# Optimization experiments

Measured on AMD Instinct MI355X. Metric: run time of the kernel, lower is better.

## Reference

```python
import jax, jax.numpy as jnp
import numpy as np

SIZE = 256  # output image is SIZE x SIZE


def lookup_table(size):
    # matches torch.meshgrid(indexing='ij') + stack + rot90
    lin = jnp.linspace(-1.0, 1.0, size)
    xx, yy = jnp.meshgrid(lin, lin, indexing='ij')
    t = jnp.stack([xx, yy], axis=-1)
    return jnp.rot90(t, 1, axes=(0, 1))  # [S,S,2]


def area2d(a, b, c):
    return (b[..., 0] - a[..., 0]) * (c[..., 1] - a[..., 1]) - (b[..., 1] - a[..., 1]) * (c[..., 0] - a[..., 0])


def face_normals(tris):
    n = jnp.cross(tris[:, 1] - tris[:, 0], tris[:, 2] - tris[:, 0])
    # NB: faithful to source: normalize by GLOBAL Frobenius norm (not per-face)
    return n / jnp.linalg.norm(n)


def vertex_normals(vertices, f):
    fn = face_normals(vertices[f])
    vn = jnp.zeros_like(vertices)
    vn = vn.at[f[:, 0]].add(fn).at[f[:, 1]].add(fn).at[f[:, 2]].add(fn)
    return vn / jnp.linalg.norm(vn)


def bilinear_sample(img, gx, gy):
    # torch.grid_sampler_2d, mode=bilinear, padding=zeros, align_corners=False
    # img: [C,H,W]; gx -> width axis, gy -> height axis, both in [-1,1]
    C, H, W = img.shape
    x = ((gx + 1.0) * W - 1.0) * 0.5
    y = ((gy + 1.0) * H - 1.0) * 0.5
    x0 = jnp.floor(x)
    y0 = jnp.floor(y)
    x1 = x0 + 1.0
    y1 = y0 + 1.0
    wx1 = x - x0
    wx0 = 1.0 - wx1
    wy1 = y - y0
    wy0 = 1.0 - wy1

    def gather(ix, iy):
        valid = (ix >= 0) & (ix <= W - 1) & (iy >= 0) & (iy <= H - 1)
        ixc = jnp.clip(ix, 0, W - 1).astype(jnp.int32)
        iyc = jnp.clip(iy, 0, H - 1).astype(jnp.int32)
        return img[:, iyc, ixc] * valid  # [C,...]

    return (gather(x0, y0) * (wx0 * wy0) + gather(x1, y0) * (wx1 * wy0)
            + gather(x0, y1) * (wx0 * wy1) + gather(x1, y1) * (wx1 * wy1))


def setup_inputs() -> dict:
    key = jax.random.key(0)
    k1, k2, k3, k4, k5, k6 = jax.random.split(key, 6)
    V, F, M = 1024, 256, 1024
    xy = jax.random.uniform(k1, (V, 2), minval=-1.0, maxval=1.0, dtype=jnp.float32)
    z = jax.random.uniform(k2, (V, 1), minval=0.5, maxval=1.5, dtype=jnp.float32)
    vertices = jnp.concatenate([xy, z], axis=1)
    faces = jax.random.randint(k3, (F, 3), 0, V, dtype=jnp.int64)
    uv = jax.random.uniform(k4, (M, 2), dtype=jnp.float32)
    uvfaces = jax.random.randint(k5, (F, 3), 0, M, dtype=jnp.int64)
    uvmap = jax.random.uniform(k6, (3, 256, 256), dtype=jnp.float32)
    return {"vertices": vertices, "faces": faces, "uv": uv, "uvfaces": uvfaces, "uvmap": uvmap}


def reference(vertices, faces, uv, uvfaces, uvmap):
    size = SIZE
    pts = lookup_table(size)                       # [S,S,2]
    uvn = uv * 2.0 - 1.0                            # init: uv*2-1
    tris = vertices[faces]                          # [F,3,3]
    z_inv = 1.0 / tris[:, :, 2:3]                   # [F,3,1]
    vn = vertex_normals(vertices, faces)[faces] * z_inv
    uvs = uvn[uvfaces] * z_inv
    tri9 = jnp.concatenate([tris, uvs, vn, z_inv], axis=2)  # [F,3,9]
    cullmask = face_normals(tris)[:, 2] > 0         # backface cull, eye=(0,0,1)

    t2 = tris[:, :, :2]
    A = area2d(t2[:, 0], t2[:, 1], t2[:, 2])        # [F] signed double-area
    valid_tri = cullmask & (A >= 1e-9)              # raster skips A < 1e-9
    Asafe = jnp.where(jnp.abs(A) < 1e-9, 1.0, A)

    px = pts[..., 0][None]                          # [1,S,S]
    py = pts[..., 1][None]

    def edge(a, c):
        # area2d(a, p, c) evaluated on the pixel grid: linear in p
        ax, ay = a[:, 0, None, None], a[:, 1, None, None]
        cx, cy = c[:, 0, None, None], c[:, 1, None, None]
        return (px - ax) * (cy - ay) - (py - ay) * (cx - ax)

    pAB = edge(t2[:, 1], t2[:, 0])                  # [F,S,S]
    pCB = edge(t2[:, 2], t2[:, 1])
    pCA = edge(t2[:, 0], t2[:, 2])
    cover = (pAB > 0) & (pCB > 0) & (pCA > 0) & valid_tri[:, None, None]

    w1 = pCB / Asafe[:, None, None]
    w2 = pCA / Asafe[:, None, None]
    w3 = 1.0 - w1 - w2
    zinv_p = (w1 * tri9[:, 0, 8, None, None] + w2 * tri9[:, 1, 8, None, None]
              + w3 * tri9[:, 2, 8, None, None])     # interpolated 1/z, [F,S,S]
    zinit = vertices[:, 2].min()                    # initial z-buffer value
    ptsZ = 1.0 / jnp.where(cover, zinv_p, 1.0)      # perspective-correct depth
    score = jnp.where(cover & (ptsZ >= zinit), ptsZ, -jnp.inf)
    # sequential loop with `ptsZ >= zbuffer` converges to the max-depth winner
    winner = jnp.argmax(score, axis=0)              # [S,S]
    hit = jnp.isfinite(jnp.max(score, axis=0))      # [S,S]

    take = lambda arr: jnp.take_along_axis(arr, winner[None], axis=0)[0]
    W1, W2, W3 = take(w1), take(w2), take(w3)       # [S,S]
    tri_w = tri9[winner]                            # [S,S,3,9]
    pts9 = (W1[..., None] * tri_w[..., 0, :] + W2[..., None] * tri_w[..., 1, :]
            + W3[..., None] * tri_w[..., 2, :])     # [S,S,9]
    Zw = 1.0 / jnp.where(hit, pts9[..., 8], 1.0)
    attrs = pts9[..., :8] * Zw[..., None]           # perspective-corrected attrs
    rgb = bilinear_sample(uvmap, attrs[..., 3], attrs[..., 4])  # [3,S,S]
    hitf = hit.astype(rgb.dtype)
    result = jnp.concatenate([rgb * hitf[None], hitf[None]], axis=0)  # [4,S,S]
    return result
```

## Files before the change

kernel.cpp:

```cpp
#include <hip/hip_runtime.h>
#include <math.h>

#define SIZE   256
#define NFACES 256
#define NVERTS 1024
#define NSPLIT 4
#define FPG    (NFACES / NSPLIT)

struct __align__(16) FaceData {
    float ax, ay, bx, by, cx, cy;
    float z0i, z1i, z2i;
    float u0x, u0y, u1x, u1y, u2x, u2y;
    float Asafe;
    float valid;
    float _pad;
};

__global__ __launch_bounds__(1024) void render_kernel(
    const float* __restrict__ vertices,
    const int*   __restrict__ faces,
    const float* __restrict__ uv,
    const int*   __restrict__ uvfaces,
    const float* __restrict__ uvmap,
    float* __restrict__ out)
{
#pragma clang fp contract(off)
    __shared__ FaceData fd[NFACES];
    __shared__ float red[1024];
    __shared__ float sh_best[NSPLIT][256];
    __shared__ int   sh_win [NSPLIT][256];

    const int t   = threadIdx.x;
    const int col = t & 255;
    const int grp = t >> 8;
    const int row = blockIdx.x;

    red[t] = vertices[3*t + 2];
    __syncthreads();
    for (int s = 512; s > 0; s >>= 1) {
        if (t < s) red[t] = fminf(red[t], red[t + s]);
        __syncthreads();
    }
    const float zinit = red[0];

    if (t < NFACES) {
        const int f  = t;
        const int i0 = faces[3*f+0], i1 = faces[3*f+1], i2 = faces[3*f+2];
        const float ax = vertices[3*i0+0], ay = vertices[3*i0+1], az = vertices[3*i0+2];
        const float bx = vertices[3*i1+0], by = vertices[3*i1+1], bz = vertices[3*i1+2];
        const float cx = vertices[3*i2+0], cy = vertices[3*i2+1], cz = vertices[3*i2+2];
        const float A = (bx-ax)*(cy-ay) - (by-ay)*(cx-ax);
        const float z0i = 1.0f/az, z1i = 1.0f/bz, z2i = 1.0f/cz;
        const int j0 = uvfaces[3*f+0], j1 = uvfaces[3*f+1], j2 = uvfaces[3*f+2];
        FaceData d;
        d.ax = ax; d.ay = ay; d.bx = bx; d.by = by; d.cx = cx; d.cy = cy;
        d.z0i = z0i; d.z1i = z1i; d.z2i = z2i;
        d.u0x = (uv[2*j0+0]*2.0f - 1.0f) * z0i;
        d.u0y = (uv[2*j0+1]*2.0f - 1.0f) * z0i;
        d.u1x = (uv[2*j1+0]*2.0f - 1.0f) * z1i;
        d.u1y = (uv[2*j1+1]*2.0f - 1.0f) * z1i;
        d.u2x = (uv[2*j2+0]*2.0f - 1.0f) * z2i;
        d.u2y = (uv[2*j2+1]*2.0f - 1.0f) * z2i;
        d.Asafe = (fabsf(A) < 1e-9f) ? 1.0f : A;
        d.valid = (A >= 1e-9f) ? 1.0f : 0.0f;
        d._pad  = 0.0f;
        fd[f] = d;
    }
    __syncthreads();

    const float px = (float)(-1.0 + (double)col         * (2.0/255.0));
    const float py = (float)(-1.0 + (double)(255 - row) * (2.0/255.0));

    float best = -INFINITY;
    int   win  = 0;
    const int f0 = grp * FPG;
    for (int f = f0; f < f0 + FPG; ++f) {
        const FaceData &d = fd[f];
        const float pAB = (px - d.bx)*(d.ay - d.by) - (py - d.by)*(d.ax - d.bx);
        const float pCB = (px - d.cx)*(d.by - d.cy) - (py - d.cy)*(d.bx - d.cx);
        const float pCA = (px - d.ax)*(d.cy - d.ay) - (py - d.ay)*(d.cx - d.ax);
        if (pAB > 0.0f && pCB > 0.0f && pCA > 0.0f && d.valid > 0.5f) {
            const float w1 = pCB / d.Asafe;
            const float w2 = pCA / d.Asafe;
            const float w3 = (1.0f - w1) - w2;
            const float zp = (w1*d.z0i + w2*d.z1i) + w3*d.z2i;
            const float z  = 1.0f / zp;
            if (z >= zinit && z > best) { best = z; win = f; }
        }
    }
    sh_best[grp][col] = best;
    sh_win [grp][col] = win;
    __syncthreads();

    if (t < 256) {
        best = -INFINITY; win = 0;
        for (int g = 0; g < NSPLIT; ++g) {
            const float z = sh_best[g][t];
            if (z > best) { best = z; win = sh_win[g][t]; }
        }

        const bool  hit = (best > -INFINITY);
        const float hf  = hit ? 1.0f : 0.0f;
        float r0 = 0.0f, r1 = 0.0f, r2 = 0.0f;

        if (hit) {
            const FaceData &d = fd[win];
            const float pCB = (px - d.cx)*(d.by - d.cy) - (py - d.cy)*(d.bx - d.cx);
            const float pCA = (px - d.ax)*(d.cy - d.ay) - (py - d.ay)*(d.cx - d.ax);
            const float w1 = pCB / d.Asafe;
            const float w2 = pCA / d.Asafe;
            const float w3 = (1.0f - w1) - w2;
            const float p3 = (w1*d.u0x + w2*d.u1x) + w3*d.u2x;
            const float p4 = (w1*d.u0y + w2*d.u1y) + w3*d.u2y;
            const float p8 = (w1*d.z0i + w2*d.z1i) + w3*d.z2i;
            const float Zw = 1.0f / p8;
            const float gx = p3 * Zw;
            const float gy = p4 * Zw;

            const float x = ((gx + 1.0f)*256.0f - 1.0f)*0.5f;
            const float y = ((gy + 1.0f)*256.0f - 1.0f)*0.5f;
            const float x0f = floorf(x), y0f = floorf(y);
            const float x1f = x0f + 1.0f, y1f = y0f + 1.0f;
            const float wx1 = x - x0f, wx0 = 1.0f - wx1;
            const float wy1 = y - y0f, wy0 = 1.0f - wy1;
            const float w00 = wx0*wy0, w10 = wx1*wy0, w01 = wx0*wy1, w11 = wx1*wy1;

            {
                const bool v = (x0f >= 0.0f) && (x0f <= 255.0f) && (y0f >= 0.0f) && (y0f <= 255.0f);
                const int ix = (int)fminf(fmaxf(x0f, 0.0f), 255.0f);
                const int iy = (int)fminf(fmaxf(y0f, 0.0f), 255.0f);
                const int o  = iy*256 + ix;
                const float g0 = v ? uvmap[o]          : 0.0f;
                const float g1 = v ? uvmap[65536 + o]  : 0.0f;
                const float g2 = v ? uvmap[131072 + o] : 0.0f;
                r0 = r0 + g0*w00; r1 = r1 + g1*w00; r2 = r2 + g2*w00;
            }
            {
                const bool v = (x1f >= 0.0f) && (x1f <= 255.0f) && (y0f >= 0.0f) && (y0f <= 255.0f);
                const int ix = (int)fminf(fmaxf(x1f, 0.0f), 255.0f);
                const int iy = (int)fminf(fmaxf(y0f, 0.0f), 255.0f);
                const int o  = iy*256 + ix;
                const float g0 = v ? uvmap[o]          : 0.0f;
                const float g1 = v ? uvmap[65536 + o]  : 0.0f;
                const float g2 = v ? uvmap[131072 + o] : 0.0f;
                r0 = r0 + g0*w10; r1 = r1 + g1*w10; r2 = r2 + g2*w10;
            }
            {
                const bool v = (x0f >= 0.0f) && (x0f <= 255.0f) && (y1f >= 0.0f) && (y1f <= 255.0f);
                const int ix = (int)fminf(fmaxf(x0f, 0.0f), 255.0f);
                const int iy = (int)fminf(fmaxf(y1f, 0.0f), 255.0f);
                const int o  = iy*256 + ix;
                const float g0 = v ? uvmap[o]          : 0.0f;
                const float g1 = v ? uvmap[65536 + o]  : 0.0f;
                const float g2 = v ? uvmap[131072 + o] : 0.0f;
                r0 = r0 + g0*w01; r1 = r1 + g1*w01; r2 = r2 + g2*w01;
            }
            {
                const bool v = (x1f >= 0.0f) && (x1f <= 255.0f) && (y1f >= 0.0f) && (y1f <= 255.0f);
                const int ix = (int)fminf(fmaxf(x1f, 0.0f), 255.0f);
                const int iy = (int)fminf(fmaxf(y1f, 0.0f), 255.0f);
                const int o  = iy*256 + ix;
                const float g0 = v ? uvmap[o]          : 0.0f;
                const float g1 = v ? uvmap[65536 + o]  : 0.0f;
                const float g2 = v ? uvmap[131072 + o] : 0.0f;
                r0 = r0 + g0*w11; r1 = r1 + g1*w11; r2 = r2 + g2*w11;
            }
        }

        const int pix = row*256 + t;
        out[           pix] = r0*hf;
        out[ 65536 +   pix] = r1*hf;
        out[131072 +   pix] = r2*hf;
        out[196608 +   pix] = hf;
    }
}

extern "C" void kernel_launch(void* const* d_in, const int* in_sizes, int n_in,
                              void* d_out, int out_size, void* d_ws, size_t ws_size,
                              hipStream_t stream) {
    const float* vertices = (const float*)d_in[0];
    const int*   faces    = (const int*)  d_in[1];
    const float* uv       = (const float*)d_in[2];
    const int*   uvfaces  = (const int*)  d_in[3];
    const float* uvmap    = (const float*)d_in[4];
    float*       out      = (float*)d_out;

    render_kernel<<<SIZE, 1024, 0, stream>>>(vertices, faces, uv, uvfaces, uvmap, out);
}
```

Baseline: 85.37 us.

## Cull faces per row by y-range and compact survivors; use wave-shuffle z-min

```diff
diff --git a/kernel.cpp b/kernel.cpp
--- a/kernel.cpp
+++ b/kernel.cpp
@@ -5,15 +5,12 @@
 #define NFACES 256
 #define NVERTS 1024
 #define NSPLIT 4
-#define FPG    (NFACES / NSPLIT)
 
 struct __align__(16) FaceData {
     float ax, ay, bx, by, cx, cy;
     float z0i, z1i, z2i;
     float u0x, u0y, u1x, u1y, u2x, u2y;
-    float Asafe;
-    float valid;
-    float _pad;
+    float A;
 };
 
 __global__ __launch_bounds__(1024) void render_kernel(
@@ -26,23 +23,33 @@
 {
 #pragma clang fp contract(off)
     __shared__ FaceData fd[NFACES];
-    __shared__ float red[1024];
     __shared__ float sh_best[NSPLIT][256];
     __shared__ int   sh_win [NSPLIT][256];
-
-    const int t   = threadIdx.x;
-    const int col = t & 255;
-    const int grp = t >> 8;
-    const int row = blockIdx.x;
-
-    red[t] = vertices[3*t + 2];
-    __syncthreads();
-    for (int s = 512; s > 0; s >>= 1) {
-        if (t < s) red[t] = fminf(red[t], red[t + s]);
-        __syncthreads();
-    }
-    const float zinit = red[0];
-
+    __shared__ float wred[16];
+    __shared__ int   wcnt[4];
+    __shared__ int   s_nv;
+
+    const int t    = threadIdx.x;
+    const int lane = t & 63;
+    const int wv   = t >> 6;
+    const int col  = t & 255;
+    const int grp  = t >> 8;
+    const int row  = blockIdx.x;
+
+    const float px = (float)(-1.0 + (double)col         * (2.0/255.0));
+    const float py = (float)(-1.0 + (double)(255 - row) * (2.0/255.0));
+
+    {
+        float m = vertices[3*t + 2];
+        for (int off = 32; off > 0; off >>= 1)
+            m = fminf(m, __shfl_down(m, off));
+        if (lane == 0) wred[wv] = m;
+    }
+
+    FaceData d;
+    bool keep = false;
+    unsigned long long bmask = 0ull;
+    int rank = 0;
     if (t < NFACES) {
         const int f  = t;
         const int i0 = faces[3*f+0], i1 = faces[3*f+1], i2 = faces[3*f+2];
@@ -50,40 +57,62 @@
         const float bx = vertices[3*i1+0], by = vertices[3*i1+1], bz = vertices[3*i1+2];
         const float cx = vertices[3*i2+0], cy = vertices[3*i2+1], cz = vertices[3*i2+2];
         const float A = (bx-ax)*(cy-ay) - (by-ay)*(cx-ax);
-        const float z0i = 1.0f/az, z1i = 1.0f/bz, z2i = 1.0f/cz;
-        const int j0 = uvfaces[3*f+0], j1 = uvfaces[3*f+1], j2 = uvfaces[3*f+2];
-        FaceData d;
-        d.ax = ax; d.ay = ay; d.bx = bx; d.by = by; d.cx = cx; d.cy = cy;
-        d.z0i = z0i; d.z1i = z1i; d.z2i = z2i;
-        d.u0x = (uv[2*j0+0]*2.0f - 1.0f) * z0i;
-        d.u0y = (uv[2*j0+1]*2.0f - 1.0f) * z0i;
-        d.u1x = (uv[2*j1+0]*2.0f - 1.0f) * z1i;
-        d.u1y = (uv[2*j1+1]*2.0f - 1.0f) * z1i;
-        d.u2x = (uv[2*j2+0]*2.0f - 1.0f) * z2i;
-        d.u2y = (uv[2*j2+1]*2.0f - 1.0f) * z2i;
-        d.Asafe = (fabsf(A) < 1e-9f) ? 1.0f : A;
-        d.valid = (A >= 1e-9f) ? 1.0f : 0.0f;
-        d._pad  = 0.0f;
-        fd[f] = d;
+        const float ymin = fminf(fminf(ay, by), cy);
+        const float ymax = fmaxf(fmaxf(ay, by), cy);
+        keep = (A >= 1e-9f) && (py > ymin - 1e-4f) && (py < ymax + 1e-4f);
+        bmask = __ballot(keep);
+        rank  = __popcll(bmask & ((1ull << lane) - 1ull));
+        if (lane == 0) wcnt[wv] = (int)__popcll(bmask);
+        if (keep) {
+            const float z0i = 1.0f/az, z1i = 1.0f/bz, z2i = 1.0f/cz;
+            const int j0 = uvfaces[3*f+0], j1 = uvfaces[3*f+1], j2 = uvfaces[3*f+2];
+            d.ax = ax; d.ay = ay; d.bx = bx; d.by = by; d.cx = cx; d.cy = cy;
+            d.z0i = z0i; d.z1i = z1i; d.z2i = z2i;
+            d.u0x = (uv[2*j0+0]*2.0f - 1.0f) * z0i;
+            d.u0y = (uv[2*j0+1]*2.0f - 1.0f) * z0i;
+            d.u1x = (uv[2*j1+0]*2.0f - 1.0f) * z1i;
+            d.u1y = (uv[2*j1+1]*2.0f - 1.0f) * z1i;
+            d.u2x = (uv[2*j2+0]*2.0f - 1.0f) * z2i;
+            d.u2y = (uv[2*j2+1]*2.0f - 1.0f) * z2i;
+            d.A = A;
+        }
     }
     __syncthreads();
 
-    const float px = (float)(-1.0 + (double)col         * (2.0/255.0));
-    const float py = (float)(-1.0 + (double)(255 - row) * (2.0/255.0));
+    float zinit;
+    {
+        float mm = wred[0];
+        #pragma unroll
+        for (int i = 1; i < 16; ++i) mm = fminf(mm, wred[i]);
+        zinit = mm;
+    }
+
+    if (t < NFACES) {
+        int base = 0;
+        #pragma unroll
+        for (int w = 0; w < 4; ++w) if (w < wv) base += wcnt[w];
+        if (keep) fd[base + rank] = d;
+        if (t == 0) s_nv = wcnt[0] + wcnt[1] + wcnt[2] + wcnt[3];
+    }
+    __syncthreads();
+
+    const int nv = s_nv;
+    const int cs = (nv + NSPLIT - 1) / NSPLIT;
+    int f0 = grp * cs;       if (f0 > nv) f0 = nv;
+    int f1 = f0 + cs;        if (f1 > nv) f1 = nv;
 
     float best = -INFINITY;
     int   win  = 0;
-    const int f0 = grp * FPG;
-    for (int f = f0; f < f0 + FPG; ++f) {
-        const FaceData &d = fd[f];
-        const float pAB = (px - d.bx)*(d.ay - d.by) - (py - d.by)*(d.ax - d.bx);
-        const float pCB = (px - d.cx)*(d.by - d.cy) - (py - d.cy)*(d.bx - d.cx);
-        const float pCA = (px - d.ax)*(d.cy - d.ay) - (py - d.ay)*(d.cx - d.ax);
-        if (pAB > 0.0f && pCB > 0.0f && pCA > 0.0f && d.valid > 0.5f) {
-            const float w1 = pCB / d.Asafe;
-            const float w2 = pCA / d.Asafe;
+    for (int f = f0; f < f1; ++f) {
+        const FaceData &c = fd[f];
+        const float pAB = (px - c.bx)*(c.ay - c.by) - (py - c.by)*(c.ax - c.bx);
+        const float pCB = (px - c.cx)*(c.by - c.cy) - (py - c.cy)*(c.bx - c.cx);
+        const float pCA = (px - c.ax)*(c.cy - c.ay) - (py - c.ay)*(c.cx - c.ax);
+        if (pAB > 0.0f && pCB > 0.0f && pCA > 0.0f) {
+            const float w1 = pCB / c.A;
+            const float w2 = pCA / c.A;
             const float w3 = (1.0f - w1) - w2;
-            const float zp = (w1*d.z0i + w2*d.z1i) + w3*d.z2i;
+            const float zp = (w1*c.z0i + w2*c.z1i) + w3*c.z2i;
             const float z  = 1.0f / zp;
             if (z >= zinit && z > best) { best = z; win = f; }
         }
@@ -94,6 +123,7 @@
 
     if (t < 256) {
         best = -INFINITY; win = 0;
+        #pragma unroll
         for (int g = 0; g < NSPLIT; ++g) {
             const float z = sh_best[g][t];
             if (z > best) { best = z; win = sh_win[g][t]; }
@@ -104,15 +134,15 @@
         float r0 = 0.0f, r1 = 0.0f, r2 = 0.0f;
 
         if (hit) {
-            const FaceData &d = fd[win];
-            const float pCB = (px - d.cx)*(d.by - d.cy) - (py - d.cy)*(d.bx - d.cx);
-            const float pCA = (px - d.ax)*(d.cy - d.ay) - (py - d.ay)*(d.cx - d.ax);
-            const float w1 = pCB / d.Asafe;
-            const float w2 = pCA / d.Asafe;
+            const FaceData &c = fd[win];
+            const float pCB = (px - c.cx)*(c.by - c.cy) - (py - c.cy)*(c.bx - c.cx);
+            const float pCA = (px - c.ax)*(c.cy - c.ay) - (py - c.ay)*(c.cx - c.ax);
+            const float w1 = pCB / c.A;
+            const float w2 = pCA / c.A;
             const float w3 = (1.0f - w1) - w2;
-            const float p3 = (w1*d.u0x + w2*d.u1x) + w3*d.u2x;
-            const float p4 = (w1*d.u0y + w2*d.u1y) + w3*d.u2y;
-            const float p8 = (w1*d.z0i + w2*d.z1i) + w3*d.z2i;
+            const float p3 = (w1*c.u0x + w2*c.u1x) + w3*c.u2x;
+            const float p4 = (w1*c.u0y + w2*c.u1y) + w3*c.u2y;
+            const float p8 = (w1*c.z0i + w2*c.z1i) + w3*c.z2i;
             const float Zw = 1.0f / p8;
             const float gx = p3 * Zw;
             const float gy = p4 * Zw;
```

New measurement: 75.31 us. 11.8% less time.

## Bin faces per row in a prep kernel and cull by column bounding box

Applied to the files above, without the earlier changes.

```diff
diff --git a/kernel.cpp b/kernel.cpp
--- a/kernel.cpp
+++ b/kernel.cpp
@@ -1,102 +1,173 @@
 #include <hip/hip_runtime.h>
 #include <math.h>
+#include <limits.h>
 
 #define SIZE   256
 #define NFACES 256
 #define NVERTS 1024
 #define NSPLIT 4
-#define FPG    (NFACES / NSPLIT)
-
-struct __align__(16) FaceData {
-    float ax, ay, bx, by, cx, cy;
-    float z0i, z1i, z2i;
-    float u0x, u0y, u1x, u1y, u2x, u2y;
-    float Asafe;
-    float valid;
-    float _pad;
-};
-
-__global__ __launch_bounds__(1024) void render_kernel(
+#define PFSZ   20
+
+
+
+__global__ __launch_bounds__(256) void prep_kernel(
     const float* __restrict__ vertices,
     const int*   __restrict__ faces,
     const float* __restrict__ uv,
     const int*   __restrict__ uvfaces,
+    float* __restrict__ fdG, float* __restrict__ zinitp,
+    int* __restrict__ rowPtr, int* __restrict__ ids)
+{
+#pragma clang fp contract(off)
+    __shared__ int   scnt[256];
+    __shared__ int   sscan[256];
+    __shared__ int   soff[256];
+    __shared__ float wred[4];
+
+    const int t    = threadIdx.x;
+    const int lane = t & 63;
+    const int wv   = t >> 6;
+
+    {
+        float m = fminf(fminf(vertices[3*t+2],       vertices[3*(t+256)+2]),
+                        fminf(vertices[3*(t+512)+2], vertices[3*(t+768)+2]));
+        for (int off = 32; off > 0; off >>= 1) m = fminf(m, __shfl_down(m, off));
+        if (lane == 0) wred[wv] = m;
+    }
+    scnt[t] = 0;
+
+    const int i0 = faces[3*t+0], i1 = faces[3*t+1], i2 = faces[3*t+2];
+    const float ax = vertices[3*i0+0], ay = vertices[3*i0+1], az = vertices[3*i0+2];
+    const float bx = vertices[3*i1+0], by = vertices[3*i1+1], bz = vertices[3*i1+2];
+    const float cx = vertices[3*i2+0], cy = vertices[3*i2+1], cz = vertices[3*i2+2];
+    const float A = (bx-ax)*(cy-ay) - (by-ay)*(cx-ax);
+    const float z0i = 1.0f/az, z1i = 1.0f/bz, z2i = 1.0f/cz;
+    const int j0 = uvfaces[3*t+0], j1 = uvfaces[3*t+1], j2 = uvfaces[3*t+2];
+    float* r = &fdG[t*PFSZ];
+    r[0]=ax; r[1]=ay; r[2]=bx; r[3]=by; r[4]=cx; r[5]=cy;
+    r[6]=z0i; r[7]=z1i; r[8]=z2i;
+    r[9]  = (uv[2*j0+0]*2.0f - 1.0f) * z0i;
+    r[10] = (uv[2*j0+1]*2.0f - 1.0f) * z0i;
+    r[11] = (uv[2*j1+0]*2.0f - 1.0f) * z1i;
+    r[12] = (uv[2*j1+1]*2.0f - 1.0f) * z1i;
+    r[13] = (uv[2*j2+0]*2.0f - 1.0f) * z2i;
+    r[14] = (uv[2*j2+1]*2.0f - 1.0f) * z2i;
+    r[15] = A;
+    r[16] = fminf(fminf(ax,bx),cx);
+    r[17] = fmaxf(fmaxf(ax,bx),cx);
+    r[18] = 0.0f; r[19] = 0.0f;
+
+    const float ymin = fminf(fminf(ay,by),cy);
+    const float ymax = fmaxf(fmaxf(ay,by),cy);
+    const bool keep = (A >= 1e-9f);
+    int r_lo = 0, r_hi = -1;
+    if (keep) {
+        r_lo = (int)floor((1.0 - ((double)ymax + 1e-4)) * 127.5) - 1;
+        r_hi = (int)ceil ((1.0 - ((double)ymin - 1e-4)) * 127.5) + 1;
+        if (r_lo < 0)   r_lo = 0;
+        if (r_hi > 255) r_hi = 255;
+    }
+    __syncthreads();
+
+    if (t == 0) zinitp[0] = fminf(fminf(wred[0],wred[1]), fminf(wred[2],wred[3]));
+
+    for (int rr = r_lo; rr <= r_hi; ++rr) atomicAdd(&scnt[rr], 1);
+    __syncthreads();
+
+    sscan[t] = scnt[t];
+    __syncthreads();
+    for (int s = 1; s < 256; s <<= 1) {
+        const int add = (t >= s) ? sscan[t - s] : 0;
+        __syncthreads();
+        sscan[t] += add;
+        __syncthreads();
+    }
+    rowPtr[t+1] = sscan[t];
+    if (t == 0) rowPtr[0] = 0;
+    soff[t] = sscan[t] - scnt[t];
+    __syncthreads();
+
+    for (int rr = r_lo; rr <= r_hi; ++rr) {
+        const int pos = atomicAdd(&soff[rr], 1);
+        ids[pos] = t;
+    }
+}
+
+__global__ __launch_bounds__(1024) void raster_kernel(
+    const float* __restrict__ fdG, const float* __restrict__ zinitp,
+    const int* __restrict__ rowPtr, const int* __restrict__ ids,
     const float* __restrict__ uvmap,
     float* __restrict__ out)
 {
 #pragma clang fp contract(off)
-    __shared__ FaceData fd[NFACES];
-    __shared__ float red[1024];
+    __shared__ float fdl[NFACES * PFSZ];
+    __shared__ int   sfid[NFACES];
     __shared__ float sh_best[NSPLIT][256];
-    __shared__ int   sh_win [NSPLIT][256];
+    __shared__ int   sh_fid [NSPLIT][256];
+    __shared__ int   sh_slot[NSPLIT][256];
 
     const int t   = threadIdx.x;
     const int col = t & 255;
     const int grp = t >> 8;
     const int row = blockIdx.x;
 
-    red[t] = vertices[3*t + 2];
-    __syncthreads();
-    for (int s = 512; s > 0; s >>= 1) {
-        if (t < s) red[t] = fminf(red[t], red[t + s]);
-        __syncthreads();
-    }
-    const float zinit = red[0];
-
-    if (t < NFACES) {
-        const int f  = t;
-        const int i0 = faces[3*f+0], i1 = faces[3*f+1], i2 = faces[3*f+2];
-        const float ax = vertices[3*i0+0], ay = vertices[3*i0+1], az = vertices[3*i0+2];
-        const float bx = vertices[3*i1+0], by = vertices[3*i1+1], bz = vertices[3*i1+2];
-        const float cx = vertices[3*i2+0], cy = vertices[3*i2+1], cz = vertices[3*i2+2];
-        const float A = (bx-ax)*(cy-ay) - (by-ay)*(cx-ax);
-        const float z0i = 1.0f/az, z1i = 1.0f/bz, z2i = 1.0f/cz;
-        const int j0 = uvfaces[3*f+0], j1 = uvfaces[3*f+1], j2 = uvfaces[3*f+2];
-        FaceData d;
-        d.ax = ax; d.ay = ay; d.bx = bx; d.by = by; d.cx = cx; d.cy = cy;
-        d.z0i = z0i; d.z1i = z1i; d.z2i = z2i;
-        d.u0x = (uv[2*j0+0]*2.0f - 1.0f) * z0i;
-        d.u0y = (uv[2*j0+1]*2.0f - 1.0f) * z0i;
-        d.u1x = (uv[2*j1+0]*2.0f - 1.0f) * z1i;
-        d.u1y = (uv[2*j1+1]*2.0f - 1.0f) * z1i;
-        d.u2x = (uv[2*j2+0]*2.0f - 1.0f) * z2i;
-        d.u2y = (uv[2*j2+1]*2.0f - 1.0f) * z2i;
-        d.Asafe = (fabsf(A) < 1e-9f) ? 1.0f : A;
-        d.valid = (A >= 1e-9f) ? 1.0f : 0.0f;
-        d._pad  = 0.0f;
-        fd[f] = d;
+    const int base = rowPtr[row];
+    const int nv   = rowPtr[row+1] - base;
+    const float zinit = zinitp[0];
+
+    for (int i = t; i < nv; i += 1024) {
+        const int f = ids[base + i];
+        sfid[i] = f;
+        const float4* src = (const float4*)&fdG[f * PFSZ];
+        float4*       dst = (float4*)&fdl[i * PFSZ];
+        dst[0] = src[0]; dst[1] = src[1]; dst[2] = src[2]; dst[3] = src[3]; dst[4] = src[4];
     }
     __syncthreads();
 
     const float px = (float)(-1.0 + (double)col         * (2.0/255.0));
     const float py = (float)(-1.0 + (double)(255 - row) * (2.0/255.0));
 
+    const int   c0   = ((t >> 6) & 3) * 64;
+    const float pxlo = (float)(-1.0 + (double)c0        * (2.0/255.0));
+    const float pxhi = (float)(-1.0 + (double)(c0 + 63) * (2.0/255.0));
+
+    const int cs = (nv + NSPLIT - 1) / NSPLIT;
+    int f0 = grp * cs; if (f0 > nv) f0 = nv;
+    int f1 = f0 + cs;  if (f1 > nv) f1 = nv;
+
     float best = -INFINITY;
-    int   win  = 0;
-    const int f0 = grp * FPG;
-    for (int f = f0; f < f0 + FPG; ++f) {
-        const FaceData &d = fd[f];
-        const float pAB = (px - d.bx)*(d.ay - d.by) - (py - d.by)*(d.ax - d.bx);
-        const float pCB = (px - d.cx)*(d.by - d.cy) - (py - d.cy)*(d.bx - d.cx);
-        const float pCA = (px - d.ax)*(d.cy - d.ay) - (py - d.ay)*(d.cx - d.ax);
-        if (pAB > 0.0f && pCB > 0.0f && pCA > 0.0f && d.valid > 0.5f) {
-            const float w1 = pCB / d.Asafe;
-            const float w2 = pCA / d.Asafe;
+    int   wfid = INT_MAX;
+    int   wslot = 0;
+    for (int i = f0; i < f1; ++i) {
+        const float* c = &fdl[i * PFSZ];
+        if (c[17] + 1e-4f < pxlo || c[16] - 1e-4f > pxhi) continue;
+        const float pAB = (px - c[2])*(c[1] - c[3]) - (py - c[3])*(c[0] - c[2]);
+        const float pCB = (px - c[4])*(c[3] - c[5]) - (py - c[5])*(c[2] - c[4]);
+        const float pCA = (px - c[0])*(c[5] - c[1]) - (py - c[1])*(c[4] - c[0]);
+        if (pAB > 0.0f && pCB > 0.0f && pCA > 0.0f) {
+            const float w1 = pCB / c[15];
+            const float w2 = pCA / c[15];
             const float w3 = (1.0f - w1) - w2;
-            const float zp = (w1*d.z0i + w2*d.z1i) + w3*d.z2i;
+            const float zp = (w1*c[6] + w2*c[7]) + w3*c[8];
             const float z  = 1.0f / zp;
-            if (z >= zinit && z > best) { best = z; win = f; }
+            if (z >= zinit) {
+                const int fid = sfid[i];
+                if (z > best || (z == best && fid < wfid)) { best = z; wfid = fid; wslot = i; }
+            }
         }
     }
     sh_best[grp][col] = best;
-    sh_win [grp][col] = win;
+    sh_fid [grp][col] = wfid;
+    sh_slot[grp][col] = wslot;
     __syncthreads();
 
     if (t < 256) {
-        best = -INFINITY; win = 0;
+        best = -INFINITY; wfid = INT_MAX; wslot = 0;
+        #pragma unroll
         for (int g = 0; g < NSPLIT; ++g) {
             const float z = sh_best[g][t];
-            if (z > best) { best = z; win = sh_win[g][t]; }
+            const int   f = sh_fid [g][t];
+            if (z > best || (z == best && f < wfid)) { best = z; wfid = f; wslot = sh_slot[g][t]; }
         }
 
         const bool  hit = (best > -INFINITY);
@@ -104,15 +175,15 @@
         float r0 = 0.0f, r1 = 0.0f, r2 = 0.0f;
 
         if (hit) {
-            const FaceData &d = fd[win];
-            const float pCB = (px - d.cx)*(d.by - d.cy) - (py - d.cy)*(d.bx - d.cx);
-            const float pCA = (px - d.ax)*(d.cy - d.ay) - (py - d.ay)*(d.cx - d.ax);
-            const float w1 = pCB / d.Asafe;
-            const float w2 = pCA / d.Asafe;
+            const float* c = &fdl[wslot * PFSZ];
+            const float pCB = (px - c[4])*(c[3] - c[5]) - (py - c[5])*(c[2] - c[4]);
+            const float pCA = (px - c[0])*(c[5] - c[1]) - (py - c[1])*(c[4] - c[0]);
+            const float w1 = pCB / c[15];
+            const float w2 = pCA / c[15];
             const float w3 = (1.0f - w1) - w2;
-            const float p3 = (w1*d.u0x + w2*d.u1x) + w3*d.u2x;
-            const float p4 = (w1*d.u0y + w2*d.u1y) + w3*d.u2y;
-            const float p8 = (w1*d.z0i + w2*d.z1i) + w3*d.z2i;
+            const float p3 = (w1*c[9]  + w2*c[11]) + w3*c[13];
+            const float p4 = (w1*c[10] + w2*c[12]) + w3*c[14];
+            const float p8 = (w1*c[6]  + w2*c[7])  + w3*c[8];
             const float Zw = 1.0f / p8;
             const float gx = p3 * Zw;
             const float gy = p4 * Zw;
@@ -185,5 +256,13 @@
     const float* uvmap    = (const float*)d_in[4];
     float*       out      = (float*)d_out;
 
-    render_kernel<<<SIZE, 1024, 0, stream>>>(vertices, faces, uv, uvfaces, uvmap, out);
+    char* ws = (char*)d_ws;
+    float* fdG    = (float*)(ws + 0);
+    float* zinitp = (float*)(ws + 20480);
+    int*   rowPtr = (int*)  (ws + 20544);
+    int*   ids    = (int*)  (ws + 22528);
+
+    prep_kernel  <<<1,   256,  0, stream>>>(vertices, faces, uv, uvfaces,
+                                            fdG, zinitp, rowPtr, ids);
+    raster_kernel<<<SIZE, 1024, 0, stream>>>(fdG, zinitp, rowPtr, ids, uvmap, out);
 }
```

Result: slower. 98.73 us (+15.6%).
